# Performance work log

Hardware: AMD Instinct MI355X
Metric: run time of the kernel (lower is better)

## Reference

```python
import jax, jax.numpy as jnp
import numpy as np

B, T, F_IN, H = 512, 512, 64, 128
BN_EPS = 1e-3  # Keras BatchNormalization default epsilon


def setup_inputs() -> dict:
    key = jax.random.key(0)
    ks = jax.random.split(key, 12)
    x = jax.random.normal(ks[0], (B, T, F_IN), dtype=jnp.float32)
    # last channel is a discrete phase index in {0,1,2}, stored as float
    state = jax.random.randint(ks[1], (B, T, 1), 0, 3).astype(jnp.float32)
    inputs = jnp.concatenate([x, state], axis=-1)  # [B, T, F_IN+1]
    s = 1.0 / np.sqrt(H)
    return {
        "inputs": inputs,
        "Wx": jax.random.normal(ks[2], (F_IN, 3 * H), dtype=jnp.float32) * s,
        "Wh": jax.random.normal(ks[3], (H, 3 * H), dtype=jnp.float32) * s,
        "b": jax.random.normal(ks[4], (2, 3 * H), dtype=jnp.float32) * 0.01,
        "W_state": jax.random.normal(ks[5], (3, H), dtype=jnp.float32),
        "w1": jax.random.normal(ks[6], (H, 64), dtype=jnp.float32) * s,
        "b1": jnp.zeros((64,), jnp.float32),
        "gamma": jnp.ones((64,), jnp.float32),
        "beta": jnp.zeros((64,), jnp.float32),
        "mean": jnp.zeros((64,), jnp.float32),
        "var": jnp.ones((64,), jnp.float32),
        "w2": jax.random.normal(ks[7], (64, 1), dtype=jnp.float32) * 0.125,
        "b2": jnp.zeros((1,), jnp.float32),
    }


def _gru_final_state(x, Wx, Wh, b):
    # Keras GRU, reset_after=True (default): separate input / recurrent biases.
    b_in, b_rec = b[0], b[1]
    xw = x @ Wx + b_in                      # [B, T, 3H] (precompute input matmuls)
    xw_t = jnp.swapaxes(xw, 0, 1)           # [T, B, 3H]
    h0 = jnp.zeros((x.shape[0], Wh.shape[0]), x.dtype)

    def step(h, xw_step):
        rec = h @ Wh + b_rec                # [B, 3H]
        xz, xr, xh = jnp.split(xw_step, 3, axis=-1)
        rz, rr, rh = jnp.split(rec, 3, axis=-1)
        z = jax.nn.sigmoid(xz + rz)
        r = jax.nn.sigmoid(xr + rr)
        hh = jnp.tanh(xh + r * rh)
        h_new = z * h + (1.0 - z) * hh
        return h_new, None

    h_final, _ = jax.lax.scan(step, h0, xw_t)
    return h_final                          # [B, H]


def reference(inputs, Wx, Wh, b, W_state, w1, b1, gamma, beta, mean, var, w2, b2):
    x = inputs[:, :, :-1]                   # [B, T, F_IN]
    state = inputs[:, :, -1]                # [B, T]
    hidden = _gru_final_state(x, Wx, Wh, b)  # [B, H]
    idx = jnp.clip(state[:, -1].astype(jnp.int32), 0, W_state.shape[0] - 1)
    hidden = hidden + W_state[idx]          # gather-add phase effect
    h = jax.nn.relu(hidden @ w1 + b1)       # dense1
    # dropout: identity in inference mode
    h = (h - mean) * jax.lax.rsqrt(var + BN_EPS) * gamma + beta  # batchnorm (inference)
    return h @ w2 + b2                      # [B, 1]
```

## Files before the change

kernel.cpp:

```cpp
#include <hip/hip_runtime.h>
#include <hip/hip_bf16.h>

#define T_SEQ   512
#define H_DIM   128
#define N3H     384
#define HSW     128
#define XS      72

typedef float f32x4 __attribute__((ext_vector_type(4)));
typedef float f32x2 __attribute__((ext_vector_type(2)));
typedef float f32x4u __attribute__((ext_vector_type(4), aligned(4)));
typedef __bf16 bf16x8 __attribute__((ext_vector_type(8)));
typedef unsigned short us8 __attribute__((ext_vector_type(8)));
typedef unsigned short us4 __attribute__((ext_vector_type(4)));

static __device__ __forceinline__ unsigned short f2bf(float f) {
    unsigned int u = __builtin_bit_cast(unsigned int, f);
    u += 0x7FFFu + ((u >> 16) & 1u);
    return (unsigned short)(u >> 16);
}

static __device__ __forceinline__ void lds_barrier() {
    asm volatile("" ::: "memory");
    __builtin_amdgcn_s_waitcnt(0xC07F);
    __builtin_amdgcn_s_barrier();
    asm volatile("" ::: "memory");
}

static __device__ __forceinline__ bf16x8 ld8(const unsigned short* p) {
    return __builtin_bit_cast(bf16x8, *(const us8*)p);
}

__global__ __launch_bounds__(512, 1) void gru_fused(
    const float* __restrict__ inputs, const float* __restrict__ Wx,
    const float* __restrict__ Wh, const float* __restrict__ bias,
    const float* __restrict__ W_state, const float* __restrict__ w1,
    const float* __restrict__ b1, const float* __restrict__ gamma,
    const float* __restrict__ beta, const float* __restrict__ mean,
    const float* __restrict__ var, const float* __restrict__ w2,
    const float* __restrict__ b2, float* __restrict__ out)
{
    __shared__ __attribute__((aligned(16))) unsigned short hb[2][16 * HSW];
    __shared__ __attribute__((aligned(16))) unsigned short xb[2][16 * XS];
    __shared__ float hf[16][H_DIM + 1];

    const int tid  = threadIdx.x;
    const int w    = tid >> 6;
    const int lane = tid & 63;
    const int m    = lane & 15;
    const int q    = lane >> 4;
    const int b0   = blockIdx.x * 16;

    const float SCL0 = -1.4426950408889634f;
    const float SCL2 =  2.8853900817779268f;

    bf16x8 whB[3][4];
    bf16x8 wxB[3][2];
    float brec[3], bin[3];
#pragma unroll
    for (int g = 0; g < 3; ++g) {
        const float s = (g < 2) ? SCL0 : SCL2;
        const int col = (8 * g + w) * 16 + m;
#pragma unroll
        for (int k = 0; k < 4; ++k) {
            us8 tmp;
#pragma unroll
            for (int j = 0; j < 8; ++j) tmp[j] = f2bf(s * Wh[(32 * k + 8 * q + j) * N3H + col]);
            whB[g][k] = __builtin_bit_cast(bf16x8, tmp);
        }
#pragma unroll
        for (int k = 0; k < 2; ++k) {
            us8 tmp;
#pragma unroll
            for (int j = 0; j < 8; ++j) tmp[j] = f2bf(s * Wx[(32 * k + 8 * q + j) * N3H + col]);
            wxB[g][k] = __builtin_bit_cast(bf16x8, tmp);
        }
        bin[g]  = s * bias[col];
        brec[g] = s * bias[N3H + col];
    }

    int hro[4], hwo[4], xro[2];
#pragma unroll
    for (int k = 0; k < 4; ++k) hro[k] = m * HSW + (((4 * k + q) ^ (m & 7)) * 8);
#pragma unroll
    for (int i = 0; i < 4; ++i) {
        const int row = 4 * q + i;
        hwo[i] = row * HSW + (((2 * w + (m >> 3)) ^ (row & 7)) * 8) + (m & 7);
    }
#pragma unroll
    for (int k = 0; k < 2; ++k) xro[k] = m * XS + 32 * k + 8 * q;

    const int sr = tid >> 4, sc = tid & 15;
    const int xwoff = sr * XS + sc * 4;
    const float* xsrc = inputs + ((size_t)(b0 + sr) * T_SEQ) * 65 + sc * 4;

    auto xpack = [&](f32x4u v) -> us4 {
        us4 r; r[0] = f2bf(v[0]); r[1] = f2bf(v[1]); r[2] = f2bf(v[2]); r[3] = f2bf(v[3]);
        return r;
    };

    {
        unsigned int* p = (unsigned int*)hb[0];
        for (int i = tid; i < 16 * HSW / 2; i += 512) p[i] = 0;
    }
    if (tid < 256) {
        f32x4u v0 = *(const f32x4u*)(xsrc + 0 * 65);
        f32x4u v1 = *(const f32x4u*)(xsrc + 1 * 65);
        *(us4*)&xb[0][xwoff] = xpack(v0);
        *(us4*)&xb[1][xwoff] = xpack(v1);
    }
    lds_barrier();

    f32x4 xwA[3], xwB[3];
    {
        bf16x8 xa[2];
#pragma unroll
        for (int k = 0; k < 2; ++k) xa[k] = ld8(&xb[0][xro[k]]);
#pragma unroll
        for (int g = 0; g < 3; ++g) {
            f32x4 acc = { bin[g], bin[g], bin[g], bin[g] };
            acc = __builtin_amdgcn_mfma_f32_16x16x32_bf16(xa[0], wxB[g][0], acc, 0, 0, 0);
            acc = __builtin_amdgcn_mfma_f32_16x16x32_bf16(xa[1], wxB[g][1], acc, 0, 0, 0);
            xwA[g] = acc;
        }
    }

    f32x4u pf0 = {}, pf1 = {};
    if (tid < 256) pf0 = *(const f32x4u*)(xsrc + 2 * 65);

    f32x4 hreg = { 0.f, 0.f, 0.f, 0.f };

    auto step = [&](int t, f32x4* xw_cur, f32x4* xw_next,
                    f32x4u& pfLoad, f32x4u& pfUse,
                    const unsigned short* hcur, unsigned short* hnxt,
                    const unsigned short* xnxt, unsigned short* xwr) {
        if (tid < 256 && t <= T_SEQ - 4) pfLoad = *(const f32x4u*)(xsrc + (t + 3) * 65);

        lds_barrier();

        bf16x8 ha[4];
#pragma unroll
        for (int k = 0; k < 4; ++k) ha[k] = ld8(&hcur[hro[k]]);
        bf16x8 xa[2];
        if (t < T_SEQ - 1) {
#pragma unroll
            for (int k = 0; k < 2; ++k) xa[k] = ld8(&xnxt[xro[k]]);
        }

        f32x4 racc[3];
#pragma unroll
        for (int g = 0; g < 3; ++g) {
            f32x4 a1 = { brec[g], brec[g], brec[g], brec[g] };
            a1 = __builtin_amdgcn_mfma_f32_16x16x32_bf16(ha[0], whB[g][0], a1, 0, 0, 0);
            a1 = __builtin_amdgcn_mfma_f32_16x16x32_bf16(ha[1], whB[g][1], a1, 0, 0, 0);
            f32x4 a2 = { 0.f, 0.f, 0.f, 0.f };
            a2 = __builtin_amdgcn_mfma_f32_16x16x32_bf16(ha[2], whB[g][2], a2, 0, 0, 0);
            a2 = __builtin_amdgcn_mfma_f32_16x16x32_bf16(ha[3], whB[g][3], a2, 0, 0, 0);
            racc[g] = a1 + a2;
        }

        f32x4 hnew;
#pragma unroll
        for (int i = 0; i < 4; ++i) {
            const float ea = __builtin_amdgcn_exp2f(xw_cur[0][i] + racc[0][i]);
            const float eb = __builtin_amdgcn_exp2f(xw_cur[1][i] + racc[1][i]);
            const float Pa = 1.0f + ea, Pb = 1.0f + eb;
            const float D  = __builtin_amdgcn_rcpf(Pa * Pb);
            const float z  = Pb * D;
            const float r  = Pa * D;
            const float u  = fmaf(r, racc[2][i], xw_cur[2][i]);
            const float ec = __builtin_amdgcn_exp2f(u);
            const float hh = fmaf(-2.0f, __builtin_amdgcn_rcpf(1.0f + ec), 1.0f);
            hnew[i] = fmaf(z, hreg[i] - hh, hh);
        }
        hreg = hnew;

        if (t < T_SEQ - 1) {
#pragma unroll
            for (int g = 0; g < 3; ++g) {
                f32x4 acc = { bin[g], bin[g], bin[g], bin[g] };
                acc = __builtin_amdgcn_mfma_f32_16x16x32_bf16(xa[0], wxB[g][0], acc, 0, 0, 0);
                acc = __builtin_amdgcn_mfma_f32_16x16x32_bf16(xa[1], wxB[g][1], acc, 0, 0, 0);
                xw_next[g] = acc;
            }
        }

#pragma unroll
        for (int i = 0; i < 4; ++i) hnxt[hwo[i]] = f2bf(hnew[i]);

        if (tid < 256 && t <= T_SEQ - 3) *(us4*)&xwr[xwoff] = xpack(pfUse);
    };

    for (int t = 0; t < T_SEQ; t += 2) {
        step(t,     xwA, xwB, pf1, pf0, hb[0], hb[1], xb[1], xb[0]);
        step(t + 1, xwB, xwA, pf0, pf1, hb[1], hb[0], xb[0], xb[1]);
    }

#pragma unroll
    for (int i = 0; i < 4; ++i)
        hf[4 * q + i][16 * w + m] = hreg[i];
    __syncthreads();

    {
        const int row = tid >> 5;
        const int c0  = (tid & 31) * 4;
        const float sf = inputs[((size_t)(b0 + row) * T_SEQ + (T_SEQ - 1)) * 65 + 64];
        int si = (int)sf;
        si = si < 0 ? 0 : (si > 2 ? 2 : si);
#pragma unroll
        for (int c = 0; c < 4; ++c)
            hf[row][c0 + c] += W_state[si * H_DIM + c0 + c];
    }
    __syncthreads();

    {
        const int row = tid >> 5;
        const int jj  = (tid & 31) * 2;
        f32x2 acc = { b1[jj], b1[jj + 1] };
        for (int k = 0; k < H_DIM; ++k) {
            const float hv = hf[row][k];
            const f32x2 wv = *(const f32x2*)(w1 + k * 64 + jj);
            acc[0] = fmaf(hv, wv[0], acc[0]);
            acc[1] = fmaf(hv, wv[1], acc[1]);
        }
        float v = 0.0f;
#pragma unroll
        for (int ii = 0; ii < 2; ++ii) {
            const int j = jj + ii;
            float a = fmaxf(acc[ii], 0.0f);
            a = (a - mean[j]) * rsqrtf(var[j] + 1e-3f) * gamma[j] + beta[j];
            v = fmaf(a, w2[j], v);
        }
        v += __shfl_down(v, 16);
        v += __shfl_down(v, 8);
        v += __shfl_down(v, 4);
        v += __shfl_down(v, 2);
        v += __shfl_down(v, 1);
        if ((tid & 31) == 0) out[b0 + row] = v + b2[0];
    }
}

extern "C" void kernel_launch(void* const* d_in, const int* in_sizes, int n_in,
                              void* d_out, int out_size, void* d_ws, size_t ws_size,
                              hipStream_t stream) {
    (void)in_sizes; (void)n_in; (void)out_size; (void)d_ws; (void)ws_size;
    const float* inputs  = (const float*)d_in[0];
    const float* Wx      = (const float*)d_in[1];
    const float* Wh      = (const float*)d_in[2];
    const float* bias    = (const float*)d_in[3];
    const float* W_state = (const float*)d_in[4];
    const float* w1      = (const float*)d_in[5];
    const float* b1      = (const float*)d_in[6];
    const float* gamma   = (const float*)d_in[7];
    const float* beta    = (const float*)d_in[8];
    const float* mean    = (const float*)d_in[9];
    const float* var     = (const float*)d_in[10];
    const float* w2      = (const float*)d_in[11];
    const float* b2      = (const float*)d_in[12];
    float* out = (float*)d_out;

    gru_fused<<<32, 512, 0, stream>>>(inputs, Wx, Wh, bias, W_state, w1, b1,
                                      gamma, beta, mean, var, w2, b2, out);
}
```

Measured before the change: 475.9 us.

## Interleave two independent batch tiles per block to hide recurrence latency

Each workgroup now processes two 16-row batch tiles (32 rows), interleaving their recurrent matmuls, gate math and input projections within each time step. The grid shrinks from 32 to 16 blocks. The goal is to fill the latency bubbles of the serial GRU dependency chain with independent work from the second tile. The cost is more work per step on each block and higher register pressure. The epilogue is adjusted to handle 32 rows with wider vector loads.

After: 807.3 us. 1.7x slower.

```diff
diff --git a/kernel.cpp b/kernel.cpp
--- a/kernel.cpp
+++ b/kernel.cpp
@@ -14,6 +14,9 @@
 typedef unsigned short us8 __attribute__((ext_vector_type(8)));
 typedef unsigned short us4 __attribute__((ext_vector_type(4)));
 
+#define SCL0 (-1.4426950408889634f)
+#define SCL2 ( 2.8853900817779268f)
+
 static __device__ __forceinline__ unsigned short f2bf(float f) {
     unsigned int u = __builtin_bit_cast(unsigned int, f);
     u += 0x7FFFu + ((u >> 16) & 1u);
@@ -31,7 +34,7 @@
     return __builtin_bit_cast(bf16x8, *(const us8*)p);
 }
 
-__global__ __launch_bounds__(512, 1) void gru_fused(
+__global__ __launch_bounds__(512, 1) void gru_fused2(
     const float* __restrict__ inputs, const float* __restrict__ Wx,
     const float* __restrict__ Wh, const float* __restrict__ bias,
     const float* __restrict__ W_state, const float* __restrict__ w1,
@@ -40,19 +43,16 @@
     const float* __restrict__ var, const float* __restrict__ w2,
     const float* __restrict__ b2, float* __restrict__ out)
 {
-    __shared__ __attribute__((aligned(16))) unsigned short hb[2][16 * HSW];
-    __shared__ __attribute__((aligned(16))) unsigned short xb[2][16 * XS];
-    __shared__ float hf[16][H_DIM + 1];
+    __shared__ __attribute__((aligned(16))) unsigned short hb[2][2][16 * HSW];
+    __shared__ __attribute__((aligned(16))) unsigned short xb[2][2][16 * XS];
+    __shared__ float hf[32][H_DIM + 1];
 
     const int tid  = threadIdx.x;
     const int w    = tid >> 6;
     const int lane = tid & 63;
     const int m    = lane & 15;
     const int q    = lane >> 4;
-    const int b0   = blockIdx.x * 16;
-
-    const float SCL0 = -1.4426950408889634f;
-    const float SCL2 =  2.8853900817779268f;
+    const int b0   = blockIdx.x * 32;
 
     bf16x8 whB[3][4];
     bf16x8 wxB[3][2];
@@ -90,9 +90,11 @@
 #pragma unroll
     for (int k = 0; k < 2; ++k) xro[k] = m * XS + 32 * k + 8 * q;
 
-    const int sr = tid >> 4, sc = tid & 15;
+    const int stile = tid >> 8;
+    const int sr    = (tid >> 4) & 15;
+    const int sc    = tid & 15;
     const int xwoff = sr * XS + sc * 4;
-    const float* xsrc = inputs + ((size_t)(b0 + sr) * T_SEQ) * 65 + sc * 4;
+    const float* xsrc = inputs + ((size_t)(b0 + stile * 16 + sr) * T_SEQ) * 65 + sc * 4;
 
     auto xpack = [&](f32x4u v) -> us4 {
         us4 r; r[0] = f2bf(v[0]); r[1] = f2bf(v[1]); r[2] = f2bf(v[2]); r[3] = f2bf(v[3]);
@@ -100,65 +102,46 @@
     };
 
     {
-        unsigned int* p = (unsigned int*)hb[0];
-        for (int i = tid; i < 16 * HSW / 2; i += 512) p[i] = 0;
-    }
-    if (tid < 256) {
+        unsigned int* p0 = (unsigned int*)hb[0][0];
+        unsigned int* p1 = (unsigned int*)hb[1][0];
+        for (int i = tid; i < 16 * HSW / 2; i += 512) { p0[i] = 0; p1[i] = 0; }
+    }
+    {
         f32x4u v0 = *(const f32x4u*)(xsrc + 0 * 65);
         f32x4u v1 = *(const f32x4u*)(xsrc + 1 * 65);
-        *(us4*)&xb[0][xwoff] = xpack(v0);
-        *(us4*)&xb[1][xwoff] = xpack(v1);
+        *(us4*)&xb[stile][0][xwoff] = xpack(v0);
+        *(us4*)&xb[stile][1][xwoff] = xpack(v1);
     }
     lds_barrier();
 
-    f32x4 xwA[3], xwB[3];
-    {
-        bf16x8 xa[2];
-#pragma unroll
-        for (int k = 0; k < 2; ++k) xa[k] = ld8(&xb[0][xro[k]]);
+    f32x4 xwA0[3], xwB0[3], xwA1[3], xwB1[3];
+    {
+        bf16x8 xa0[2], xa1[2];
+#pragma unroll
+        for (int k = 0; k < 2; ++k) {
+            xa0[k] = ld8(&xb[0][0][xro[k]]);
+            xa1[k] = ld8(&xb[1][0][xro[k]]);
+        }
 #pragma unroll
         for (int g = 0; g < 3; ++g) {
-            f32x4 acc = { bin[g], bin[g], bin[g], bin[g] };
-            acc = __builtin_amdgcn_mfma_f32_16x16x32_bf16(xa[0], wxB[g][0], acc, 0, 0, 0);
-            acc = __builtin_amdgcn_mfma_f32_16x16x32_bf16(xa[1], wxB[g][1], acc, 0, 0, 0);
-            xwA[g] = acc;
+            f32x4 a0 = { bin[g], bin[g], bin[g], bin[g] };
+            a0 = __builtin_amdgcn_mfma_f32_16x16x32_bf16(xa0[0], wxB[g][0], a0, 0, 0, 0);
+            a0 = __builtin_amdgcn_mfma_f32_16x16x32_bf16(xa0[1], wxB[g][1], a0, 0, 0, 0);
+            xwA0[g] = a0;
+            f32x4 a1 = { bin[g], bin[g], bin[g], bin[g] };
+            a1 = __builtin_amdgcn_mfma_f32_16x16x32_bf16(xa1[0], wxB[g][0], a1, 0, 0, 0);
+            a1 = __builtin_amdgcn_mfma_f32_16x16x32_bf16(xa1[1], wxB[g][1], a1, 0, 0, 0);
+            xwA1[g] = a1;
         }
     }
 
     f32x4u pf0 = {}, pf1 = {};
-    if (tid < 256) pf0 = *(const f32x4u*)(xsrc + 2 * 65);
-
-    f32x4 hreg = { 0.f, 0.f, 0.f, 0.f };
-
-    auto step = [&](int t, f32x4* xw_cur, f32x4* xw_next,
-                    f32x4u& pfLoad, f32x4u& pfUse,
-                    const unsigned short* hcur, unsigned short* hnxt,
-                    const unsigned short* xnxt, unsigned short* xwr) {
-        if (tid < 256 && t <= T_SEQ - 4) pfLoad = *(const f32x4u*)(xsrc + (t + 3) * 65);
-
-        lds_barrier();
-
-        bf16x8 ha[4];
-#pragma unroll
-        for (int k = 0; k < 4; ++k) ha[k] = ld8(&hcur[hro[k]]);
-        bf16x8 xa[2];
-        if (t < T_SEQ - 1) {
-#pragma unroll
-            for (int k = 0; k < 2; ++k) xa[k] = ld8(&xnxt[xro[k]]);
-        }
-
-        f32x4 racc[3];
-#pragma unroll
-        for (int g = 0; g < 3; ++g) {
-            f32x4 a1 = { brec[g], brec[g], brec[g], brec[g] };
-            a1 = __builtin_amdgcn_mfma_f32_16x16x32_bf16(ha[0], whB[g][0], a1, 0, 0, 0);
-            a1 = __builtin_amdgcn_mfma_f32_16x16x32_bf16(ha[1], whB[g][1], a1, 0, 0, 0);
-            f32x4 a2 = { 0.f, 0.f, 0.f, 0.f };
-            a2 = __builtin_amdgcn_mfma_f32_16x16x32_bf16(ha[2], whB[g][2], a2, 0, 0, 0);
-            a2 = __builtin_amdgcn_mfma_f32_16x16x32_bf16(ha[3], whB[g][3], a2, 0, 0, 0);
-            racc[g] = a1 + a2;
-        }
-
+    pf0 = *(const f32x4u*)(xsrc + 2 * 65);
+
+    f32x4 hreg0 = { 0.f, 0.f, 0.f, 0.f };
+    f32x4 hreg1 = { 0.f, 0.f, 0.f, 0.f };
+
+    auto gates = [&](const f32x4* racc, const f32x4* xw_cur, f32x4& hreg) {
         f32x4 hnew;
 #pragma unroll
         for (int i = 0; i < 4; ++i) {
@@ -174,69 +157,134 @@
             hnew[i] = fmaf(z, hreg[i] - hh, hh);
         }
         hreg = hnew;
-
+    };
+
+    auto recmm = [&](const bf16x8* ha, f32x4* racc) {
+#pragma unroll
+        for (int g = 0; g < 3; ++g) {
+            f32x4 a1 = { brec[g], brec[g], brec[g], brec[g] };
+            a1 = __builtin_amdgcn_mfma_f32_16x16x32_bf16(ha[0], whB[g][0], a1, 0, 0, 0);
+            a1 = __builtin_amdgcn_mfma_f32_16x16x32_bf16(ha[1], whB[g][1], a1, 0, 0, 0);
+            f32x4 a2 = { 0.f, 0.f, 0.f, 0.f };
+            a2 = __builtin_amdgcn_mfma_f32_16x16x32_bf16(ha[2], whB[g][2], a2, 0, 0, 0);
+            a2 = __builtin_amdgcn_mfma_f32_16x16x32_bf16(ha[3], whB[g][3], a2, 0, 0, 0);
+            racc[g] = a1 + a2;
+        }
+    };
+
+    auto xwmm = [&](const bf16x8* xa, f32x4* xw_next) {
+#pragma unroll
+        for (int g = 0; g < 3; ++g) {
+            f32x4 acc = { bin[g], bin[g], bin[g], bin[g] };
+            acc = __builtin_amdgcn_mfma_f32_16x16x32_bf16(xa[0], wxB[g][0], acc, 0, 0, 0);
+            acc = __builtin_amdgcn_mfma_f32_16x16x32_bf16(xa[1], wxB[g][1], acc, 0, 0, 0);
+            xw_next[g] = acc;
+        }
+    };
+
+    auto step = [&](int t,
+                    f32x4* xw_cur0, f32x4* xw_next0,
+                    f32x4* xw_cur1, f32x4* xw_next1,
+                    f32x4u& pfLoad, f32x4u& pfUse,
+                    const unsigned short* hcur0, unsigned short* hnxt0,
+                    const unsigned short* hcur1, unsigned short* hnxt1,
+                    const unsigned short* xnxt0, const unsigned short* xnxt1,
+                    unsigned short* xwr0, unsigned short* xwr1) {
+        if (t <= T_SEQ - 4) pfLoad = *(const f32x4u*)(xsrc + (t + 3) * 65);
+
+        lds_barrier();
+
+        bf16x8 ha0[4], ha1[4];
+#pragma unroll
+        for (int k = 0; k < 4; ++k) ha0[k] = ld8(&hcur0[hro[k]]);
+#pragma unroll
+        for (int k = 0; k < 4; ++k) ha1[k] = ld8(&hcur1[hro[k]]);
+        bf16x8 xa0[2], xa1[2];
         if (t < T_SEQ - 1) {
 #pragma unroll
-            for (int g = 0; g < 3; ++g) {
-                f32x4 acc = { bin[g], bin[g], bin[g], bin[g] };
-                acc = __builtin_amdgcn_mfma_f32_16x16x32_bf16(xa[0], wxB[g][0], acc, 0, 0, 0);
-                acc = __builtin_amdgcn_mfma_f32_16x16x32_bf16(xa[1], wxB[g][1], acc, 0, 0, 0);
-                xw_next[g] = acc;
+            for (int k = 0; k < 2; ++k) {
+                xa0[k] = ld8(&xnxt0[xro[k]]);
+                xa1[k] = ld8(&xnxt1[xro[k]]);
             }
         }
 
-#pragma unroll
-        for (int i = 0; i < 4; ++i) hnxt[hwo[i]] = f2bf(hnew[i]);
-
-        if (tid < 256 && t <= T_SEQ - 3) *(us4*)&xwr[xwoff] = xpack(pfUse);
+        f32x4 racc0[3], racc1[3];
+        recmm(ha0, racc0);
+        recmm(ha1, racc1);
+
+        gates(racc0, xw_cur0, hreg0);
+#pragma unroll
+        for (int i = 0; i < 4; ++i) hnxt0[hwo[i]] = f2bf(hreg0[i]);
+        gates(racc1, xw_cur1, hreg1);
+#pragma unroll
+        for (int i = 0; i < 4; ++i) hnxt1[hwo[i]] = f2bf(hreg1[i]);
+
+        if (t < T_SEQ - 1) {
+            xwmm(xa0, xw_next0);
+            xwmm(xa1, xw_next1);
+        }
+
+        if (t <= T_SEQ - 3) {
+            unsigned short* xwr = stile ? xwr1 : xwr0;
+            *(us4*)&xwr[xwoff] = xpack(pfUse);
+        }
     };
 
     for (int t = 0; t < T_SEQ; t += 2) {
-        step(t,     xwA, xwB, pf1, pf0, hb[0], hb[1], xb[1], xb[0]);
-        step(t + 1, xwB, xwA, pf0, pf1, hb[1], hb[0], xb[0], xb[1]);
-    }
-
-#pragma unroll
-    for (int i = 0; i < 4; ++i)
-        hf[4 * q + i][16 * w + m] = hreg[i];
+        step(t,     xwA0, xwB0, xwA1, xwB1, pf1, pf0,
+             hb[0][0], hb[0][1], hb[1][0], hb[1][1],
+             xb[0][1], xb[1][1], xb[0][0], xb[1][0]);
+        step(t + 1, xwB0, xwA0, xwB1, xwA1, pf0, pf1,
+             hb[0][1], hb[0][0], hb[1][1], hb[1][0],
+             xb[0][0], xb[1][0], xb[0][1], xb[1][1]);
+    }
+
+#pragma unroll
+    for (int i = 0; i < 4; ++i) {
+        hf[4 * q + i][16 * w + m]      = hreg0[i];
+        hf[16 + 4 * q + i][16 * w + m] = hreg1[i];
+    }
     __syncthreads();
 
     {
-        const int row = tid >> 5;
-        const int c0  = (tid & 31) * 4;
+        const int row = tid >> 4;
+        const int c0  = (tid & 15) * 8;
         const float sf = inputs[((size_t)(b0 + row) * T_SEQ + (T_SEQ - 1)) * 65 + 64];
         int si = (int)sf;
         si = si < 0 ? 0 : (si > 2 ? 2 : si);
 #pragma unroll
-        for (int c = 0; c < 4; ++c)
+        for (int c = 0; c < 8; ++c)
             hf[row][c0 + c] += W_state[si * H_DIM + c0 + c];
     }
     __syncthreads();
 
     {
-        const int row = tid >> 5;
-        const int jj  = (tid & 31) * 2;
-        f32x2 acc = { b1[jj], b1[jj + 1] };
+        const int row = tid >> 4;
+        const int c4  = (tid & 15) * 4;
+        f32x4 acc = *(const f32x4*)(b1 + c4);
         for (int k = 0; k < H_DIM; ++k) {
             const float hv = hf[row][k];
-            const f32x2 wv = *(const f32x2*)(w1 + k * 64 + jj);
-            acc[0] = fmaf(hv, wv[0], acc[0]);
-            acc[1] = fmaf(hv, wv[1], acc[1]);
-        }
+            const f32x4 wv = *(const f32x4*)(w1 + k * 64 + c4);
+#pragma unroll
+            for (int ii = 0; ii < 4; ++ii) acc[ii] = fmaf(hv, wv[ii], acc[ii]);
+        }
+        const f32x4 mv = *(const f32x4*)(mean + c4);
+        const f32x4 vv = *(const f32x4*)(var + c4);
+        const f32x4 gv = *(const f32x4*)(gamma + c4);
+        const f32x4 bv = *(const f32x4*)(beta + c4);
+        const f32x4 w2v = *(const f32x4*)(w2 + c4);
         float v = 0.0f;
 #pragma unroll
-        for (int ii = 0; ii < 2; ++ii) {
-            const int j = jj + ii;
+        for (int ii = 0; ii < 4; ++ii) {
             float a = fmaxf(acc[ii], 0.0f);
-            a = (a - mean[j]) * rsqrtf(var[j] + 1e-3f) * gamma[j] + beta[j];
-            v = fmaf(a, w2[j], v);
-        }
-        v += __shfl_down(v, 16);
+            a = (a - mv[ii]) * rsqrtf(vv[ii] + 1e-3f) * gv[ii] + bv[ii];
+            v = fmaf(a, w2v[ii], v);
+        }
         v += __shfl_down(v, 8);
         v += __shfl_down(v, 4);
         v += __shfl_down(v, 2);
         v += __shfl_down(v, 1);
-        if ((tid & 31) == 0) out[b0 + row] = v + b2[0];
+        if ((tid & 15) == 0) out[b0 + row] = v + b2[0];
     }
 }
 
@@ -259,6 +307,6 @@
     const float* b2      = (const float*)d_in[12];
     float* out = (float*)d_out;
 
-    gru_fused<<<32, 512, 0, stream>>>(inputs, Wx, Wh, bias, W_state, w1, b1,
-                                      gamma, beta, mean, var, w2, b2, out);
-}
+    gru_fused2<<<16, 512, 0, stream>>>(inputs, Wx, Wh, bias, W_state, w1, b1,
+                                       gamma, beta, mean, var, w2, b2, out);
+}
```

## Load x fragments directly into registers and fold input projection into recurrent MFMA accumulator

Applied to the files above, without the earlier changes.

Removes the LDS staging buffer for x: each lane loads its own fp32 x slice from global memory two steps ahead and packs it to bf16 by truncation with a perm instruction instead of round-to-nearest. The z/r input projections, with both biases pre-summed, now seed the recurrent MFMA accumulator, which drops the separate split-accumulator adds. The next step's x projection MFMAs are moved before the gate math so they can overlap it. This cuts LDS traffic and conversion work per step, at the cost of more global loads per lane, more registers, and slightly lower precision from truncating x.

After: 635.5 us. 33.5% more time.

```diff
diff --git a/kernel.cpp b/kernel.cpp
--- a/kernel.cpp
+++ b/kernel.cpp
@@ -5,19 +5,27 @@
 #define H_DIM   128
 #define N3H     384
 #define HSW     128
-#define XS      72
 
 typedef float f32x4 __attribute__((ext_vector_type(4)));
 typedef float f32x2 __attribute__((ext_vector_type(2)));
 typedef float f32x4u __attribute__((ext_vector_type(4), aligned(4)));
 typedef __bf16 bf16x8 __attribute__((ext_vector_type(8)));
 typedef unsigned short us8 __attribute__((ext_vector_type(8)));
-typedef unsigned short us4 __attribute__((ext_vector_type(4)));
+typedef unsigned int u32x4 __attribute__((ext_vector_type(4)));
+
+#define SCL0 (-1.4426950408889634f)
+#define SCL2 ( 2.8853900817779268f)
 
 static __device__ __forceinline__ unsigned short f2bf(float f) {
     unsigned int u = __builtin_bit_cast(unsigned int, f);
     u += 0x7FFFu + ((u >> 16) & 1u);
     return (unsigned short)(u >> 16);
+}
+
+static __device__ __forceinline__ unsigned int pk_trunc(float a, float b) {
+    return __builtin_amdgcn_perm(__builtin_bit_cast(unsigned int, a),
+                                 __builtin_bit_cast(unsigned int, b),
+                                 0x03020706u);
 }
 
 static __device__ __forceinline__ void lds_barrier() {
@@ -41,7 +49,6 @@
     const float* __restrict__ b2, float* __restrict__ out)
 {
     __shared__ __attribute__((aligned(16))) unsigned short hb[2][16 * HSW];
-    __shared__ __attribute__((aligned(16))) unsigned short xb[2][16 * XS];
     __shared__ float hf[16][H_DIM + 1];
 
     const int tid  = threadIdx.x;
@@ -51,12 +58,10 @@
     const int q    = lane >> 4;
     const int b0   = blockIdx.x * 16;
 
-    const float SCL0 = -1.4426950408889634f;
-    const float SCL2 =  2.8853900817779268f;
-
     bf16x8 whB[3][4];
     bf16x8 wxB[3][2];
-    float brec[3], bin[3];
+    float bin[3];
+    float brec2;
 #pragma unroll
     for (int g = 0; g < 3; ++g) {
         const float s = (g < 2) ? SCL0 : SCL2;
@@ -75,11 +80,11 @@
             for (int j = 0; j < 8; ++j) tmp[j] = f2bf(s * Wx[(32 * k + 8 * q + j) * N3H + col]);
             wxB[g][k] = __builtin_bit_cast(bf16x8, tmp);
         }
-        bin[g]  = s * bias[col];
-        brec[g] = s * bias[N3H + col];
-    }
-
-    int hro[4], hwo[4], xro[2];
+        bin[g] = (g < 2) ? s * (bias[col] + bias[N3H + col]) : s * bias[col];
+    }
+    brec2 = SCL2 * bias[N3H + (16 + w) * 16 + m];
+
+    int hro[4], hwo[4];
 #pragma unroll
     for (int k = 0; k < 4; ++k) hro[k] = m * HSW + (((4 * k + q) ^ (m & 7)) * 8);
 #pragma unroll
@@ -87,35 +92,39 @@
         const int row = 4 * q + i;
         hwo[i] = row * HSW + (((2 * w + (m >> 3)) ^ (row & 7)) * 8) + (m & 7);
     }
-#pragma unroll
-    for (int k = 0; k < 2; ++k) xro[k] = m * XS + 32 * k + 8 * q;
-
-    const int sr = tid >> 4, sc = tid & 15;
-    const int xwoff = sr * XS + sc * 4;
-    const float* xsrc = inputs + ((size_t)(b0 + sr) * T_SEQ) * 65 + sc * 4;
-
-    auto xpack = [&](f32x4u v) -> us4 {
-        us4 r; r[0] = f2bf(v[0]); r[1] = f2bf(v[1]); r[2] = f2bf(v[2]); r[3] = f2bf(v[3]);
-        return r;
+
+    const float* xlane = inputs + ((size_t)(b0 + m) * T_SEQ) * 65 + 8 * q;
+    auto ldx = [&](int t, f32x4u* R) {
+        const float* p = xlane + (size_t)t * 65;
+        R[0] = *(const f32x4u*)p;
+        R[1] = *(const f32x4u*)(p + 4);
+        R[2] = *(const f32x4u*)(p + 32);
+        R[3] = *(const f32x4u*)(p + 36);
+    };
+    auto mkfrag = [&](const f32x4u* R, bf16x8* xa) {
+#pragma unroll
+        for (int k = 0; k < 2; ++k) {
+            u32x4 p;
+            p[0] = pk_trunc(R[2 * k][0], R[2 * k][1]);
+            p[1] = pk_trunc(R[2 * k][2], R[2 * k][3]);
+            p[2] = pk_trunc(R[2 * k + 1][0], R[2 * k + 1][1]);
+            p[3] = pk_trunc(R[2 * k + 1][2], R[2 * k + 1][3]);
+            xa[k] = __builtin_bit_cast(bf16x8, p);
+        }
     };
 
     {
         unsigned int* p = (unsigned int*)hb[0];
         for (int i = tid; i < 16 * HSW / 2; i += 512) p[i] = 0;
     }
-    if (tid < 256) {
-        f32x4u v0 = *(const f32x4u*)(xsrc + 0 * 65);
-        f32x4u v1 = *(const f32x4u*)(xsrc + 1 * 65);
-        *(us4*)&xb[0][xwoff] = xpack(v0);
-        *(us4*)&xb[1][xwoff] = xpack(v1);
-    }
-    lds_barrier();
-
+
+    f32x4u R0[4], R1[4];
+    ldx(0, R0);
+    ldx(1, R1);
     f32x4 xwA[3], xwB[3];
     {
         bf16x8 xa[2];
-#pragma unroll
-        for (int k = 0; k < 2; ++k) xa[k] = ld8(&xb[0][xro[k]]);
+        mkfrag(R0, xa);
 #pragma unroll
         for (int g = 0; g < 3; ++g) {
             f32x4 acc = { bin[g], bin[g], bin[g], bin[g] };
@@ -124,46 +133,49 @@
             xwA[g] = acc;
         }
     }
-
-    f32x4u pf0 = {}, pf1 = {};
-    if (tid < 256) pf0 = *(const f32x4u*)(xsrc + 2 * 65);
+    lds_barrier();
 
     f32x4 hreg = { 0.f, 0.f, 0.f, 0.f };
 
-    auto step = [&](int t, f32x4* xw_cur, f32x4* xw_next,
-                    f32x4u& pfLoad, f32x4u& pfUse,
+    auto step = [&](int t, f32x4u* Rload, f32x4u* Rconv,
+                    f32x4* xw_cur, f32x4* xw_next,
                     const unsigned short* hcur, unsigned short* hnxt,
-                    const unsigned short* xnxt, unsigned short* xwr) {
-        if (tid < 256 && t <= T_SEQ - 4) pfLoad = *(const f32x4u*)(xsrc + (t + 3) * 65);
-
-        lds_barrier();
+                    bool first) {
+        if (t + 2 < T_SEQ) ldx(t + 2, Rload);
+
+        if (!first) lds_barrier();
 
         bf16x8 ha[4];
 #pragma unroll
         for (int k = 0; k < 4; ++k) ha[k] = ld8(&hcur[hro[k]]);
-        bf16x8 xa[2];
-        if (t < T_SEQ - 1) {
-#pragma unroll
-            for (int k = 0; k < 2; ++k) xa[k] = ld8(&xnxt[xro[k]]);
-        }
 
         f32x4 racc[3];
 #pragma unroll
         for (int g = 0; g < 3; ++g) {
-            f32x4 a1 = { brec[g], brec[g], brec[g], brec[g] };
-            a1 = __builtin_amdgcn_mfma_f32_16x16x32_bf16(ha[0], whB[g][0], a1, 0, 0, 0);
-            a1 = __builtin_amdgcn_mfma_f32_16x16x32_bf16(ha[1], whB[g][1], a1, 0, 0, 0);
-            f32x4 a2 = { 0.f, 0.f, 0.f, 0.f };
-            a2 = __builtin_amdgcn_mfma_f32_16x16x32_bf16(ha[2], whB[g][2], a2, 0, 0, 0);
-            a2 = __builtin_amdgcn_mfma_f32_16x16x32_bf16(ha[3], whB[g][3], a2, 0, 0, 0);
-            racc[g] = a1 + a2;
+            f32x4 acc = (g < 2) ? xw_cur[g] : f32x4{ brec2, brec2, brec2, brec2 };
+#pragma unroll
+            for (int k = 0; k < 4; ++k)
+                acc = __builtin_amdgcn_mfma_f32_16x16x32_bf16(ha[k], whB[g][k], acc, 0, 0, 0);
+            racc[g] = acc;
+        }
+
+        if (t + 1 < T_SEQ) {
+            bf16x8 xa[2];
+            mkfrag(Rconv, xa);
+#pragma unroll
+            for (int g = 0; g < 3; ++g) {
+                f32x4 acc = { bin[g], bin[g], bin[g], bin[g] };
+                acc = __builtin_amdgcn_mfma_f32_16x16x32_bf16(xa[0], wxB[g][0], acc, 0, 0, 0);
+                acc = __builtin_amdgcn_mfma_f32_16x16x32_bf16(xa[1], wxB[g][1], acc, 0, 0, 0);
+                xw_next[g] = acc;
+            }
         }
 
         f32x4 hnew;
 #pragma unroll
         for (int i = 0; i < 4; ++i) {
-            const float ea = __builtin_amdgcn_exp2f(xw_cur[0][i] + racc[0][i]);
-            const float eb = __builtin_amdgcn_exp2f(xw_cur[1][i] + racc[1][i]);
+            const float ea = __builtin_amdgcn_exp2f(racc[0][i]);
+            const float eb = __builtin_amdgcn_exp2f(racc[1][i]);
             const float Pa = 1.0f + ea, Pb = 1.0f + eb;
             const float D  = __builtin_amdgcn_rcpf(Pa * Pb);
             const float z  = Pb * D;
@@ -175,26 +187,16 @@
         }
         hreg = hnew;
 
-        if (t < T_SEQ - 1) {
-#pragma unroll
-            for (int g = 0; g < 3; ++g) {
-                f32x4 acc = { bin[g], bin[g], bin[g], bin[g] };
-                acc = __builtin_amdgcn_mfma_f32_16x16x32_bf16(xa[0], wxB[g][0], acc, 0, 0, 0);
-                acc = __builtin_amdgcn_mfma_f32_16x16x32_bf16(xa[1], wxB[g][1], acc, 0, 0, 0);
-                xw_next[g] = acc;
-            }
-        }
-
 #pragma unroll
         for (int i = 0; i < 4; ++i) hnxt[hwo[i]] = f2bf(hnew[i]);
-
-        if (tid < 256 && t <= T_SEQ - 3) *(us4*)&xwr[xwoff] = xpack(pfUse);
     };
 
-    for (int t = 0; t < T_SEQ; t += 2) {
-        step(t,     xwA, xwB, pf1, pf0, hb[0], hb[1], xb[1], xb[0]);
-        step(t + 1, xwB, xwA, pf0, pf1, hb[1], hb[0], xb[0], xb[1]);
-    }
+    step(0, R0, R1, xwA, xwB, hb[0], hb[1], true);
+    for (int t = 1; t < T_SEQ - 1; t += 2) {
+        step(t,     R1, R0, xwB, xwA, hb[1], hb[0], false);
+        step(t + 1, R0, R1, xwA, xwB, hb[0], hb[1], false);
+    }
+    step(T_SEQ - 1, R1, R0, xwB, xwA, hb[1], hb[0], false);
 
 #pragma unroll
     for (int i = 0; i < 4; ++i)
```
